# Kernel optimization log

Measured on AMD Instinct MI355X. Metric: run time of the kernel, lower is better.

Reference implementation:

```python
import jax, jax.numpy as jnp
import numpy as np

N, T, C = 8, 2048, 1024   # batch, seq_len, n_embd (== num_cls)
NUM_CLS = 1024
LID, TL = 6, 12


def setup_inputs() -> dict:
    key = jax.random.key(0)
    ks = jax.random.split(key, 5)
    s = 1.0 / np.sqrt(C)
    x = jax.random.normal(ks[0], (N, T, C), jnp.float32)
    Wk = jax.random.normal(ks[1], (C, C), jnp.float32) * s
    Wv = jax.random.normal(ks[2], (C, C), jnp.float32) * s
    Wr = jax.random.normal(ks[3], (C, C), jnp.float32) * s
    Wo = jax.random.normal(ks[4], (NUM_CLS, C), jnp.float32) * s
    # faithful time-parameter initialization from __init__
    r0 = LID / (TL - 1)            # ratio_0_to_1
    r1 = 1.0 - LID / TL            # ratio_1_to_almost0
    ddd = (np.arange(C, dtype=np.float32) / C).reshape(1, 1, C)
    time_mix_k = jnp.asarray(ddd ** r1)
    time_mix_v = jnp.asarray(ddd ** r1 + 0.3 * r0)
    time_mix_r = jnp.asarray(ddd ** (0.5 * r1))
    time_decay = jnp.zeros((C,), jnp.float32)                 # decay_speed init
    time_first = jnp.full((C,), np.log(0.3), jnp.float32)
    last_x = jnp.zeros((N, 1, C), jnp.float32)                # init_x repeated
    state = jnp.zeros((N, 3, 1, C), jnp.float32)              # init_state repeated
    return {"x": x, "it": 0, "Wk": Wk, "Wv": Wv, "Wr": Wr, "Wo": Wo,
            "time_mix_k": time_mix_k, "time_mix_v": time_mix_v,
            "time_mix_r": time_mix_r, "time_decay": time_decay,
            "time_first": time_first, "last_x": last_x, "state": state}


def _wkv_with_eps(w, u, k, v, state):
    """Numerically-stabilized RWKV wkv scan. k,v: (N,T,C); state: (N,3,1,C)."""
    alpha = state[:, 0, -1]  # (N,C)
    beta = state[:, 1, -1]
    eps = state[:, 2, -1]

    def step(carry, kv):
        a, b, e = carry
        kt, vt = kv                      # each (N,C)
        ukt = u + kt
        tau = jnp.maximum(ukt, e)
        e1 = jnp.exp(e - tau)
        e2 = jnp.exp(ukt - tau)
        wkv_t = (e1 * a + e2 * vt) / (e1 * b + e2)
        w_eps = e - w
        e_n = jnp.maximum(w_eps, kt)
        e1n = jnp.exp(w_eps - e_n)
        e2n = jnp.exp(kt - e_n)
        return (e1n * a + e2n * vt, e1n * b + e2n, e_n), wkv_t

    kT = jnp.swapaxes(k, 0, 1)  # (T,N,C)
    vT = jnp.swapaxes(v, 0, 1)
    (alpha, beta, eps), wkv = jax.lax.scan(step, (alpha, beta, eps), (kT, vT))
    wkv = jnp.swapaxes(wkv, 0, 1)  # (N,T,C)
    last_state = jnp.stack([alpha, beta, eps], axis=1)[:, :, None, :]  # (N,3,1,C)
    return wkv, last_state


def reference(x, it, Wk, Wv, Wr, Wo, time_mix_k, time_mix_v, time_mix_r,
              time_decay, time_first, last_x, state):
    # time-mix blend (last_x = init_x zeros, broadcast over T as in the source)
    k = (x * time_mix_k + last_x * (1.0 - time_mix_k)) @ Wk.T
    v = (x * time_mix_v + last_x * (1.0 - time_mix_v)) @ Wv.T
    r = (x * time_mix_r + last_x * (1.0 - time_mix_r)) @ Wr.T
    sr = jax.nn.sigmoid(r)
    w = jnp.exp(time_decay)
    u = time_first
    wkv, _last_state = _wkv_with_eps(w, u, k, v, state)
    rwkv = (wkv * sr) @ Wo.T  # (N,T,NUM_CLS)
    return rwkv
```

## Files before the change

kernel.cpp:

```cpp
#include <hip/hip_runtime.h>
#include <hip/hip_bf16.h>
#include <stdint.h>


typedef float f4 __attribute__((ext_vector_type(4)));
typedef short bh8 __attribute__((ext_vector_type(8)));
typedef unsigned int u32;
typedef unsigned short u16;

__device__ __forceinline__ u32 cvt2bf(float a, float b) {
    __hip_bfloat162 h = __float22bfloat162_rn(make_float2(a, b));
    u32 u; __builtin_memcpy(&u, &h, 4); return u;
}
__device__ __forceinline__ float b2f(u16 u) {
    u32 x = (u32)u << 16; float f; __builtin_memcpy(&f, &x, 4); return f;
}
__device__ __forceinline__ u16 f2b(float f) {
    __hip_bfloat16 h = __float2bfloat16(f);
    u16 u; __builtin_memcpy(&u, &h, 2); return u;
}
__device__ __forceinline__ void gld_lds16(const void* g, void* l) {
    __builtin_amdgcn_global_load_lds(
        (const __attribute__((address_space(1))) u32*)g,
        (__attribute__((address_space(3))) u32*)l, 16, 0, 0);
}

__device__ __forceinline__ void gemm_core(
    const u16* __restrict__ A, const u16* __restrict__ B,
    int m0, int n0, u16* As, u16* Bs, f4 (&acc)[4][4])
{
    const int tid  = threadIdx.x;
    const int w    = tid >> 6;
    const int lane = tid & 63;

    const int srow = w * 32 + (lane >> 2);
    const int slot = lane & 3;
    const int chk  = slot ^ ((srow >> 1) & 3);
    const u16* gA0 = A + (size_t)(m0 + srow) * 1024 + chk * 8;
    const u16* gA1 = gA0 + (size_t)16 * 1024;
    const u16* gB0 = B + (size_t)(n0 + srow) * 1024 + chk * 8;
    const u16* gB1 = gB0 + (size_t)16 * 1024;
    u16* lA0 = As + (w * 32) * 32;
    u16* lA1 = lA0 + 16 * 32;
    u16* lB0 = Bs + (w * 32) * 32;
    u16* lB1 = lB0 + 16 * 32;

    const int fr   = lane & 15;
    const int quad = lane >> 4;
    const int wm = (w & 1) * 64;
    const int wn = (w >> 1) * 64;
    const int sp = quad ^ ((fr >> 1) & 3);
    const int aoff = (wm + fr) * 32 + sp * 8;
    const int boff = (wn + fr) * 32 + sp * 8;

    for (int kk = 0; kk < 1024; kk += 32) {
        gld_lds16(gA0 + kk, lA0);
        gld_lds16(gA1 + kk, lA1);
        gld_lds16(gB0 + kk, lB0);
        gld_lds16(gB1 + kk, lB1);
        __syncthreads();
        bh8 af[4], bf[4];
#pragma unroll
        for (int i = 0; i < 4; i++) af[i] = *(const bh8*)(As + aoff + i * 16 * 32);
#pragma unroll
        for (int j = 0; j < 4; j++) bf[j] = *(const bh8*)(Bs + boff + j * 16 * 32);
#pragma unroll
        for (int i = 0; i < 4; i++)
#pragma unroll
            for (int j = 0; j < 4; j++)
                acc[i][j] = __builtin_amdgcn_mfma_f32_16x16x32_bf16(af[i], bf[j], acc[i][j], 0, 0, 0);
        __syncthreads();
    }
}

__global__ __launch_bounds__(256, 4) void gemm_kvr(
    const u16* __restrict__ A, const u16* __restrict__ Wall, const float* __restrict__ bias,
    u16* __restrict__ Kb, u16* __restrict__ Vb, u16* __restrict__ SRb)
{
    __shared__ __align__(16) char pool[33792];
    u16* As = (u16*)pool;
    u16* Bs = (u16*)(pool + 8192);

    const int proj = blockIdx.x >> 3;
    const int n0 = (blockIdx.x & 7) * 128;
    const int m0 = blockIdx.y * 128;
    const u16* B = Wall + (size_t)proj * 1048576;

    f4 acc[4][4];
#pragma unroll
    for (int i = 0; i < 4; i++)
#pragma unroll
        for (int j = 0; j < 4; j++) { f4 z = {0.f, 0.f, 0.f, 0.f}; acc[i][j] = z; }
    gemm_core(A, B, m0, n0, As, Bs, acc);

    u16* Y = proj == 0 ? Kb : (proj == 1 ? Vb : SRb);
    const int lane = threadIdx.x & 63;
    const int w = threadIdx.x >> 6;
    const int fr = lane & 15, quad = lane >> 4;
    const int wm = (w & 1) * 64, wn = (w >> 1) * 64;
    const int rb = quad * 4;
    const int batch = m0 >> 11;
    float bv[4];
#pragma unroll
    for (int j = 0; j < 4; j++) bv[j] = bias[proj * 8192 + batch * 1024 + n0 + wn + j * 16 + fr];

    u16* S = (u16*)pool;
#pragma unroll
    for (int i = 0; i < 4; i++)
#pragma unroll
        for (int j = 0; j < 4; j++)
#pragma unroll
            for (int r = 0; r < 4; r++) {
                float v = acc[i][j][r] + bv[j];
                if (proj == 2) v = __fdividef(1.0f, 1.0f + __expf(-v));
                int row = wm + i * 16 + rb + r;
                int col = wn + j * 16 + fr;
                S[row * 132 + col] = f2b(v);
            }
    __syncthreads();
    const int ch = lane & 15;
#pragma unroll
    for (int t = 0; t < 8; t++) {
        int lrow = w * 32 + t * 4 + (lane >> 4);
        const u16* p = S + lrow * 132 + ch * 8;
        uint2 lo = *(const uint2*)p;
        uint2 hi = *(const uint2*)(p + 4);
        uint4 val = make_uint4(lo.x, lo.y, hi.x, hi.y);
        *(uint4*)(Y + (size_t)(m0 + lrow) * 1024 + n0 + ch * 8) = val;
    }
}

__global__ __launch_bounds__(256, 4) void gemm_out(
    const u16* __restrict__ A, const u16* __restrict__ B, float* __restrict__ Y)
{
    __shared__ __align__(16) char pool[33792];
    u16* As = (u16*)pool;
    u16* Bs = (u16*)(pool + 8192);
    const int n0 = blockIdx.x * 128;
    const int m0 = blockIdx.y * 128;
    f4 acc[4][4];
#pragma unroll
    for (int i = 0; i < 4; i++)
#pragma unroll
        for (int j = 0; j < 4; j++) { f4 z = {0.f, 0.f, 0.f, 0.f}; acc[i][j] = z; }
    gemm_core(A, B, m0, n0, As, Bs, acc);

    const int lane = threadIdx.x & 63;
    const int w = threadIdx.x >> 6;
    const int fr = lane & 15, quad = lane >> 4;
    const int wn = (w >> 1) * 64;
    const int rb = quad * 4;
    float* Sf = (float*)pool;
#pragma unroll
    for (int i = 0; i < 4; i++) {
        __syncthreads();
#pragma unroll
        for (int j = 0; j < 4; j++)
#pragma unroll
            for (int r = 0; r < 4; r++) {
                int lrow = (w & 1) * 16 + rb + r;
                Sf[lrow * 132 + wn + j * 16 + fr] = acc[i][j][r];
            }
        __syncthreads();
#pragma unroll
        for (int t = 0; t < 4; t++) {
            int lrow = w * 8 + t * 2 + (lane >> 5);
            int ch = lane & 31;
            f4 val = *(const f4*)(Sf + lrow * 132 + ch * 4);
            int g = m0 + ((lrow >> 4) << 6) + i * 16 + (lrow & 15);
            *(f4*)(Y + (size_t)g * 1024 + n0 + ch * 4) = val;
        }
    }
}

__global__ __launch_bounds__(256) void prep_all(
    const float* __restrict__ x, const float* __restrict__ lastx,
    const float* __restrict__ Wk, const float* __restrict__ Wv,
    const float* __restrict__ Wr, const float* __restrict__ Wo,
    const float* __restrict__ tmk, const float* __restrict__ tmv, const float* __restrict__ tmr,
    u16* __restrict__ xb, u16* __restrict__ Wall, float* __restrict__ bias)
{
    int b = blockIdx.x;
    if (b < 16384) {
        int e = (b * 256 + threadIdx.x) << 2;
        f4 v = *(const f4*)(x + e);
        *(uint2*)(xb + e) = make_uint2(cvt2bf(v.x, v.y), cvt2bf(v.z, v.w));
    } else if (b < 20480) {
        int e = ((b - 16384) * 256 + threadIdx.x) << 2;
        int wid = e >> 20;
        int off = e & 1048575;
        int c = e & 1023;
        const float* src = wid == 0 ? Wk : (wid == 1 ? Wv : (wid == 2 ? Wr : Wo));
        f4 v = *(const f4*)(src + off);
        if (wid < 3) {
            const float* m = wid == 0 ? tmk : (wid == 1 ? tmv : tmr);
            v = v * *(const f4*)(m + c);
        }
        *(uint2*)(Wall + e) = make_uint2(cvt2bf(v.x, v.y), cvt2bf(v.z, v.w));
    } else {
        int wid = (b - 20480) * 4 + (threadIdx.x >> 6);
        int lane = threadIdx.x & 63;
        int proj = wid >> 10;
        int n = wid & 1023;
        const float* W = proj == 0 ? Wk : (proj == 1 ? Wv : Wr);
        const float* m = proj == 0 ? tmk : (proj == 1 ? tmv : tmr);
        float acc[8];
#pragma unroll
        for (int bb = 0; bb < 8; bb++) acc[bb] = 0.f;
        for (int c = lane; c < 1024; c += 64) {
            float wc = W[n * 1024 + c] * (1.0f - m[c]);
#pragma unroll
            for (int bb = 0; bb < 8; bb++) acc[bb] = fmaf(lastx[bb * 1024 + c], wc, acc[bb]);
        }
#pragma unroll
        for (int bb = 0; bb < 8; bb++) {
            float v = acc[bb];
#pragma unroll
            for (int sh = 32; sh >= 1; sh >>= 1) v += __shfl_xor(v, sh);
            if (lane == 0) bias[proj * 8192 + bb * 1024 + n] = v;
        }
    }
}

__global__ __launch_bounds__(256) void wkv_pass1(
    const u16* __restrict__ Kp, const u16* __restrict__ Vp,
    const float* __restrict__ tdec,
    float* __restrict__ Ca, float* __restrict__ Cb, float* __restrict__ Ce)
{
    int tid = blockIdx.x * 256 + threadIdx.x;
    int c = (tid & 511) << 1;
    int chunk = (tid >> 9) & 63;
    int n = tid >> 15;
    float w0 = __expf(tdec[c]), w1 = __expf(tdec[c + 1]);
    int base = (n * 2048 + chunk * 32) * 1024 + c;
    float a0 = 0.f, b0 = 0.f, e0 = -1e30f;
    float a1 = 0.f, b1 = 0.f, e1 = -1e30f;
#pragma unroll 4
    for (int i = 0; i < 32; i++) {
        u32 ku = *(const u32*)(Kp + base + (i << 10));
        u32 vu = *(const u32*)(Vp + base + (i << 10));
        float k0 = b2f((u16)ku), k1 = b2f((u16)(ku >> 16));
        float v0 = b2f((u16)vu), v1 = b2f((u16)(vu >> 16));
        float en0 = fmaxf(e0 - w0, k0);
        float f10 = __expf(e0 - w0 - en0), f20 = __expf(k0 - en0);
        a0 = fmaf(f10, a0, f20 * v0); b0 = fmaf(f10, b0, f20); e0 = en0;
        float en1 = fmaxf(e1 - w1, k1);
        float f11 = __expf(e1 - w1 - en1), f21 = __expf(k1 - en1);
        a1 = fmaf(f11, a1, f21 * v1); b1 = fmaf(f11, b1, f21); e1 = en1;
    }
    int oidx = ((n * 64 + chunk) << 10) + c;
    *(float2*)(Ca + oidx) = make_float2(a0, a1);
    *(float2*)(Cb + oidx) = make_float2(b0, b1);
    *(float2*)(Ce + oidx) = make_float2(e0, e1);
}

__global__ __launch_bounds__(256) void wkv_pass2(
    const float* __restrict__ state, const float* __restrict__ tdec,
    float* Ca, float* Cb, float* Ce)
{
    int tid = blockIdx.x * 256 + threadIdx.x;
    int c = tid & 1023;
    int n = tid >> 10;
    float a = state[(n * 3 + 0) * 1024 + c];
    float b = state[(n * 3 + 1) * 1024 + c];
    float e = state[(n * 3 + 2) * 1024 + c];
    float wL = __expf(tdec[c]) * 32.0f;
    for (int ch = 0; ch < 64; ++ch) {
        int idx = ((n * 64 + ch) << 10) + c;
        float ca = Ca[idx], cb = Cb[idx], ce = Ce[idx];
        Ca[idx] = a; Cb[idx] = b; Ce[idx] = e;
        float en = fmaxf(e - wL, ce);
        float f1 = __expf(e - wL - en);
        float f2 = __expf(ce - en);
        a = fmaf(f1, a, f2 * ca);
        b = fmaf(f1, b, f2 * cb);
        e = en;
    }
}

__global__ __launch_bounds__(256) void wkv_pass3(
    const u16* __restrict__ Kp, const u16* __restrict__ Vp, const u16* __restrict__ SRp,
    const float* __restrict__ Sa, const float* __restrict__ Sb, const float* __restrict__ Se,
    const float* __restrict__ tfirst, const float* __restrict__ tdec,
    u16* __restrict__ Pp)
{
    int tid = blockIdx.x * 256 + threadIdx.x;
    int c = (tid & 511) << 1;
    int chunk = (tid >> 9) & 63;
    int n = tid >> 15;
    int sidx = ((n * 64 + chunk) << 10) + c;
    float a0 = Sa[sidx], b0 = Sb[sidx], e0 = Se[sidx];
    float a1 = Sa[sidx + 1], b1 = Sb[sidx + 1], e1 = Se[sidx + 1];
    float u0 = tfirst[c], u1 = tfirst[c + 1];
    float w0 = __expf(tdec[c]), w1 = __expf(tdec[c + 1]);
    int base = (n * 2048 + chunk * 32) * 1024 + c;
#pragma unroll 2
    for (int i = 0; i < 32; i++) {
        u32 ku = *(const u32*)(Kp + base + (i << 10));
        u32 vu = *(const u32*)(Vp + base + (i << 10));
        u32 su = *(const u32*)(SRp + base + (i << 10));
        float k0 = b2f((u16)ku), k1 = b2f((u16)(ku >> 16));
        float v0 = b2f((u16)vu), v1 = b2f((u16)(vu >> 16));
        float s0 = b2f((u16)su), s1 = b2f((u16)(su >> 16));
        float t0 = fmaxf(u0 + k0, e0);
        float x10 = __expf(e0 - t0), x20 = __expf(u0 + k0 - t0);
        float wkv0 = __fdividef(fmaf(x10, a0, x20 * v0), fmaf(x10, b0, x20));
        float t1 = fmaxf(u1 + k1, e1);
        float x11 = __expf(e1 - t1), x21 = __expf(u1 + k1 - t1);
        float wkv1 = __fdividef(fmaf(x11, a1, x21 * v1), fmaf(x11, b1, x21));
        *(u32*)(Pp + base + (i << 10)) = (u32)f2b(wkv0 * s0) | ((u32)f2b(wkv1 * s1) << 16);
        float en0 = fmaxf(e0 - w0, k0);
        float f10 = __expf(e0 - w0 - en0), f20 = __expf(k0 - en0);
        a0 = fmaf(f10, a0, f20 * v0); b0 = fmaf(f10, b0, f20); e0 = en0;
        float en1 = fmaxf(e1 - w1, k1);
        float f11 = __expf(e1 - w1 - en1), f21 = __expf(k1 - en1);
        a1 = fmaf(f11, a1, f21 * v1); b1 = fmaf(f11, b1, f21); e1 = en1;
    }
}

extern "C" void kernel_launch(void* const* d_in, const int* in_sizes, int n_in,
                              void* d_out, int out_size, void* d_ws, size_t ws_size,
                              hipStream_t stream) {
    const float* x      = (const float*)d_in[0];
    const float* Wk     = (const float*)d_in[2];
    const float* Wv     = (const float*)d_in[3];
    const float* Wr     = (const float*)d_in[4];
    const float* Wo     = (const float*)d_in[5];
    const float* tmk    = (const float*)d_in[6];
    const float* tmv    = (const float*)d_in[7];
    const float* tmr    = (const float*)d_in[8];
    const float* tdec   = (const float*)d_in[9];
    const float* tfirst = (const float*)d_in[10];
    const float* lastx  = (const float*)d_in[11];
    const float* state  = (const float*)d_in[12];
    float* out = (float*)d_out;

    const size_t MB = 1024ull * 1024ull;
    char* ws = (char*)d_ws;
    u16* Kb   = (u16*)(ws);
    u16* Vb   = (u16*)(ws + 32 * MB);
    u16* SRb  = (u16*)(ws + 64 * MB);
    u16* xb   = (u16*)(ws + 96 * MB);
    u16* Wall = (u16*)(ws + 128 * MB);
    float* bias = (float*)(ws + 136 * MB);
    float* Ca = (float*)(ws + 137 * MB);
    float* Cb = (float*)(ws + 139 * MB);
    float* Ce = (float*)(ws + 141 * MB);
    u16* Pb = xb;

    dim3 blk(256);
    prep_all<<<21248, blk, 0, stream>>>(x, lastx, Wk, Wv, Wr, Wo, tmk, tmv, tmr, xb, Wall, bias);
    gemm_kvr<<<dim3(24, 128), blk, 0, stream>>>(xb, Wall, bias, Kb, Vb, SRb);
    wkv_pass1<<<1024, blk, 0, stream>>>(Kb, Vb, tdec, Ca, Cb, Ce);
    wkv_pass2<<<32, blk, 0, stream>>>(state, tdec, Ca, Cb, Ce);
    wkv_pass3<<<1024, blk, 0, stream>>>(Kb, Vb, SRb, Ca, Cb, Ce, tfirst, tdec, Pb);
    gemm_out<<<dim3(8, 128), blk, 0, stream>>>(Pb, Wall + 3145728, out);
}
```

Before: 387.1 us.

## Compute K, V, R projections in one block sharing the A tile

The fused K/V/R projection kernel now has each block load the activation tile once and multiply it against all three weight matrices, keeping three accumulator sets. This removes the threefold reload of the A tile and cuts the grid from 24x128 to 8x128 blocks. In exchange it triples accumulator registers (launch bounds lowered to 2 blocks per SM) and puts more LDS traffic on each block, which lowers occupancy and parallelism.

Measured after the change: 368.1 us. 1.05x faster.

```diff
diff --git a/kernel.cpp b/kernel.cpp
--- a/kernel.cpp
+++ b/kernel.cpp
@@ -25,14 +25,120 @@
         (__attribute__((address_space(3))) u32*)l, 16, 0, 0);
 }
 
-__device__ __forceinline__ void gemm_core(
-    const u16* __restrict__ A, const u16* __restrict__ B,
-    int m0, int n0, u16* As, u16* Bs, f4 (&acc)[4][4])
-{
+__global__ __launch_bounds__(256, 2) void gemm_kvr(
+    const u16* __restrict__ A, const u16* __restrict__ Wall, const float* __restrict__ bias,
+    u16* __restrict__ Kb, u16* __restrict__ Vb, u16* __restrict__ SRb)
+{
+    __shared__ __align__(16) char pool[33792];
+    u16* As = (u16*)pool;
+
+    const int n0 = blockIdx.x * 128;
+    const int m0 = blockIdx.y * 128;
+
     const int tid  = threadIdx.x;
     const int w    = tid >> 6;
     const int lane = tid & 63;
 
+    const int srow = w * 32 + (lane >> 2);
+    const int slot = lane & 3;
+    const int chk  = slot ^ ((srow >> 1) & 3);
+    const u16* gA0 = A + (size_t)(m0 + srow) * 1024 + chk * 8;
+    const u16* gA1 = gA0 + (size_t)16 * 1024;
+    const u16* gW0 = Wall + (size_t)(n0 + srow) * 1024 + chk * 8;
+    const u16* gW1 = gW0 + (size_t)16 * 1024;
+    u16* lA0 = As + (w * 32) * 32;
+    u16* lA1 = lA0 + 16 * 32;
+
+    const int fr   = lane & 15;
+    const int quad = lane >> 4;
+    const int wm = (w & 1) * 64;
+    const int wn = (w >> 1) * 64;
+    const int sp = quad ^ ((fr >> 1) & 3);
+    const int aoff = (wm + fr) * 32 + sp * 8;
+    const int boff = (wn + fr) * 32 + sp * 8;
+
+    f4 acc[3][4][4];
+#pragma unroll
+    for (int p = 0; p < 3; p++)
+#pragma unroll
+        for (int i = 0; i < 4; i++)
+#pragma unroll
+            for (int j = 0; j < 4; j++) { f4 z = {0.f, 0.f, 0.f, 0.f}; acc[p][i][j] = z; }
+
+    for (int kk = 0; kk < 1024; kk += 32) {
+        gld_lds16(gA0 + kk, lA0);
+        gld_lds16(gA1 + kk, lA1);
+#pragma unroll
+        for (int p = 0; p < 3; p++) {
+            u16* lB0 = (u16*)(pool + 8192 + p * 8192) + (w * 32) * 32;
+            gld_lds16(gW0 + (size_t)p * 1048576 + kk, lB0);
+            gld_lds16(gW1 + (size_t)p * 1048576 + kk, lB0 + 16 * 32);
+        }
+        __syncthreads();
+        bh8 af[4];
+#pragma unroll
+        for (int i = 0; i < 4; i++) af[i] = *(const bh8*)(As + aoff + i * 16 * 32);
+#pragma unroll
+        for (int p = 0; p < 3; p++) {
+            const u16* Bs = (const u16*)(pool + 8192 + p * 8192);
+            bh8 bf[4];
+#pragma unroll
+            for (int j = 0; j < 4; j++) bf[j] = *(const bh8*)(Bs + boff + j * 16 * 32);
+#pragma unroll
+            for (int i = 0; i < 4; i++)
+#pragma unroll
+                for (int j = 0; j < 4; j++)
+                    acc[p][i][j] = __builtin_amdgcn_mfma_f32_16x16x32_bf16(af[i], bf[j], acc[p][i][j], 0, 0, 0);
+        }
+        __syncthreads();
+    }
+
+    const int rb = quad * 4;
+    const int batch = m0 >> 11;
+    u16* S = (u16*)pool;
+    const int ch = lane & 15;
+#pragma unroll
+    for (int p = 0; p < 3; p++) {
+        float bv[4];
+#pragma unroll
+        for (int j = 0; j < 4; j++) bv[j] = bias[p * 8192 + batch * 1024 + n0 + wn + j * 16 + fr];
+        if (p) __syncthreads();
+#pragma unroll
+        for (int i = 0; i < 4; i++)
+#pragma unroll
+            for (int j = 0; j < 4; j++)
+#pragma unroll
+                for (int r = 0; r < 4; r++) {
+                    float v = acc[p][i][j][r] + bv[j];
+                    if (p == 2) v = __fdividef(1.0f, 1.0f + __expf(-v));
+                    S[(wm + i * 16 + rb + r) * 132 + wn + j * 16 + fr] = f2b(v);
+                }
+        __syncthreads();
+        u16* Y = p == 0 ? Kb : (p == 1 ? Vb : SRb);
+#pragma unroll
+        for (int t = 0; t < 8; t++) {
+            int lrow = w * 32 + t * 4 + (lane >> 4);
+            const u16* ptr = S + lrow * 132 + ch * 8;
+            uint2 lo = *(const uint2*)ptr;
+            uint2 hi = *(const uint2*)(ptr + 4);
+            uint4 val = make_uint4(lo.x, lo.y, hi.x, hi.y);
+            *(uint4*)(Y + (size_t)(m0 + lrow) * 1024 + n0 + ch * 8) = val;
+        }
+    }
+}
+
+__global__ __launch_bounds__(256, 4) void gemm_out(
+    const u16* __restrict__ A, const u16* __restrict__ B, float* __restrict__ Y)
+{
+    __shared__ __align__(16) char pool[33792];
+    u16* As = (u16*)pool;
+    u16* Bs = (u16*)(pool + 8192);
+    const int n0 = blockIdx.x * 128;
+    const int m0 = blockIdx.y * 128;
+
+    const int tid  = threadIdx.x;
+    const int w    = tid >> 6;
+    const int lane = tid & 63;
     const int srow = w * 32 + (lane >> 2);
     const int slot = lane & 3;
     const int chk  = slot ^ ((srow >> 1) & 3);
@@ -53,6 +159,12 @@
     const int aoff = (wm + fr) * 32 + sp * 8;
     const int boff = (wn + fr) * 32 + sp * 8;
 
+    f4 acc[4][4];
+#pragma unroll
+    for (int i = 0; i < 4; i++)
+#pragma unroll
+        for (int j = 0; j < 4; j++) { f4 z = {0.f, 0.f, 0.f, 0.f}; acc[i][j] = z; }
+
     for (int kk = 0; kk < 1024; kk += 32) {
         gld_lds16(gA0 + kk, lA0);
         gld_lds16(gA1 + kk, lA1);
@@ -71,84 +183,7 @@
                 acc[i][j] = __builtin_amdgcn_mfma_f32_16x16x32_bf16(af[i], bf[j], acc[i][j], 0, 0, 0);
         __syncthreads();
     }
-}
-
-__global__ __launch_bounds__(256, 4) void gemm_kvr(
-    const u16* __restrict__ A, const u16* __restrict__ Wall, const float* __restrict__ bias,
-    u16* __restrict__ Kb, u16* __restrict__ Vb, u16* __restrict__ SRb)
-{
-    __shared__ __align__(16) char pool[33792];
-    u16* As = (u16*)pool;
-    u16* Bs = (u16*)(pool + 8192);
-
-    const int proj = blockIdx.x >> 3;
-    const int n0 = (blockIdx.x & 7) * 128;
-    const int m0 = blockIdx.y * 128;
-    const u16* B = Wall + (size_t)proj * 1048576;
-
-    f4 acc[4][4];
-#pragma unroll
-    for (int i = 0; i < 4; i++)
-#pragma unroll
-        for (int j = 0; j < 4; j++) { f4 z = {0.f, 0.f, 0.f, 0.f}; acc[i][j] = z; }
-    gemm_core(A, B, m0, n0, As, Bs, acc);
-
-    u16* Y = proj == 0 ? Kb : (proj == 1 ? Vb : SRb);
-    const int lane = threadIdx.x & 63;
-    const int w = threadIdx.x >> 6;
-    const int fr = lane & 15, quad = lane >> 4;
-    const int wm = (w & 1) * 64, wn = (w >> 1) * 64;
-    const int rb = quad * 4;
-    const int batch = m0 >> 11;
-    float bv[4];
-#pragma unroll
-    for (int j = 0; j < 4; j++) bv[j] = bias[proj * 8192 + batch * 1024 + n0 + wn + j * 16 + fr];
-
-    u16* S = (u16*)pool;
-#pragma unroll
-    for (int i = 0; i < 4; i++)
-#pragma unroll
-        for (int j = 0; j < 4; j++)
-#pragma unroll
-            for (int r = 0; r < 4; r++) {
-                float v = acc[i][j][r] + bv[j];
-                if (proj == 2) v = __fdividef(1.0f, 1.0f + __expf(-v));
-                int row = wm + i * 16 + rb + r;
-                int col = wn + j * 16 + fr;
-                S[row * 132 + col] = f2b(v);
-            }
-    __syncthreads();
-    const int ch = lane & 15;
-#pragma unroll
-    for (int t = 0; t < 8; t++) {
-        int lrow = w * 32 + t * 4 + (lane >> 4);
-        const u16* p = S + lrow * 132 + ch * 8;
-        uint2 lo = *(const uint2*)p;
-        uint2 hi = *(const uint2*)(p + 4);
-        uint4 val = make_uint4(lo.x, lo.y, hi.x, hi.y);
-        *(uint4*)(Y + (size_t)(m0 + lrow) * 1024 + n0 + ch * 8) = val;
-    }
-}
-
-__global__ __launch_bounds__(256, 4) void gemm_out(
-    const u16* __restrict__ A, const u16* __restrict__ B, float* __restrict__ Y)
-{
-    __shared__ __align__(16) char pool[33792];
-    u16* As = (u16*)pool;
-    u16* Bs = (u16*)(pool + 8192);
-    const int n0 = blockIdx.x * 128;
-    const int m0 = blockIdx.y * 128;
-    f4 acc[4][4];
-#pragma unroll
-    for (int i = 0; i < 4; i++)
-#pragma unroll
-        for (int j = 0; j < 4; j++) { f4 z = {0.f, 0.f, 0.f, 0.f}; acc[i][j] = z; }
-    gemm_core(A, B, m0, n0, As, Bs, acc);
-
-    const int lane = threadIdx.x & 63;
-    const int w = threadIdx.x >> 6;
-    const int fr = lane & 15, quad = lane >> 4;
-    const int wn = (w >> 1) * 64;
+
     const int rb = quad * 4;
     float* Sf = (float*)pool;
 #pragma unroll
@@ -350,7 +385,7 @@
 
     dim3 blk(256);
     prep_all<<<21248, blk, 0, stream>>>(x, lastx, Wk, Wv, Wr, Wo, tmk, tmv, tmr, xb, Wall, bias);
-    gemm_kvr<<<dim3(24, 128), blk, 0, stream>>>(xb, Wall, bias, Kb, Vb, SRb);
+    gemm_kvr<<<dim3(8, 128), blk, 0, stream>>>(xb, Wall, bias, Kb, Vb, SRb);
     wkv_pass1<<<1024, blk, 0, stream>>>(Kb, Vb, tdec, Ca, Cb, Ce);
     wkv_pass2<<<32, blk, 0, stream>>>(state, tdec, Ca, Cb, Ce);
     wkv_pass3<<<1024, blk, 0, stream>>>(Kb, Vb, SRb, Ca, Cb, Ce, tfirst, tdec, Pb);
```
